# Performance work log

Hardware: AMD Instinct MI355X
Metric: run time of the kernel (lower is better)

The kernel has to match this reference:

```python
import jax, jax.numpy as jnp
import numpy as np

KH, KW = 3, 3
STRIDE = 1
PADDING = 1
CIN, COUT = 64, 64


def setup_inputs() -> dict:
    key = jax.random.key(0)
    kx, kw, kb = jax.random.split(key, 3)
    x = jax.random.normal(kx, (16, CIN, 112, 112), dtype=jnp.float32)
    # Kaiming-uniform style init, matching the torch module
    fan = CIN * KH * KW
    gain = np.sqrt(2.0)
    bound_w = np.sqrt(3.0) * gain / np.sqrt(fan)
    weights = jax.random.uniform(kw, (COUT, CIN, KH, KW), dtype=jnp.float32,
                                 minval=-bound_w, maxval=bound_w)
    bound_b = 1.0 / np.sqrt(fan)
    bias = jax.random.uniform(kb, (COUT,), dtype=jnp.float32,
                              minval=-bound_b, maxval=bound_b)
    return {"x": x, "weights": weights, "bias": bias}


def reference(x, weights, bias):
    # Equivalent to F.unfold + GEMM: a standard cross-correlation conv.
    # x: (N, C, H, W), weights: (F, C, KH, KW) -> out: (N, F, H', W')
    out = jax.lax.conv_general_dilated(
        x, weights,
        window_strides=(STRIDE, STRIDE),
        padding=((PADDING, PADDING), (PADDING, PADDING)),
        dimension_numbers=("NCHW", "OIHW", "NCHW"),
    )
    return out + bias[None, :, None, None]
```

## Files before the change

### kernel.cpp

```cpp
#include <hip/hip_runtime.h>


typedef __attribute__((ext_vector_type(8))) short bf16x8;
typedef __attribute__((ext_vector_type(4))) float f32x4;

#define CIN 64
#define COUT 64
#define HH 112
#define WW 112
#define ROWS 2
#define TILES 7
#define STRIPH (ROWS * TILES)
#define NPL 8
#define WCMAX 66
#define PLANE (8 * WCMAX * 8)
#define LDS_SHORTS (NPL * PLANE)

__device__ __forceinline__ int ladr(int pl, int oct, int w) {
    return ((pl * 8 + oct) * WCMAX + w) * 8;
}

__device__ __forceinline__ unsigned short f2bf(float f) {
    unsigned u = __builtin_bit_cast(unsigned, f);
    u += 0x7FFFu + ((u >> 16) & 1u);
    return (unsigned short)(u >> 16);
}

#if __has_builtin(__builtin_amdgcn_cvt_pk_bf16_f32)
__device__ __forceinline__ unsigned pk2bf(float a, float b) {
    typedef __attribute__((ext_vector_type(2))) __bf16 bf16x2;
    bf16x2 r = __builtin_amdgcn_cvt_pk_bf16_f32(a, b);
    return __builtin_bit_cast(unsigned, r);
}
#else
__device__ __forceinline__ unsigned pk2bf(float a, float b) {
    return (unsigned)f2bf(a) | ((unsigned)f2bf(b) << 16);
}
#endif

__global__ void conv_wprep(const float* __restrict__ w, short* __restrict__ wbf) {
    int i = blockIdx.x * 256 + threadIdx.x;
    int j = i & 7;
    int f = (i >> 3) & 63;
    int koct = (i >> 9) & 3;
    int cb = (i >> 11) & 1;
    int t = i >> 12;
    int c = cb * 32 + koct * 8 + j;
    int ky = t / 3, kx = t - ky * 3;
    wbf[i] = (short)f2bf(w[((f * CIN + c) * 3 + ky) * 3 + kx]);
}

struct StageRegs {
    float v[8][4];
    float hv;
};

__device__ __forceinline__ void stage_load(const float* __restrict__ x, int tid,
                                           int n, int c0, int W4N, int gce,
                                           int row0, StageRegs& sr)
{
    const int re  = tid >> 7;
    const int oct = (tid >> 4) & 7;
    const int w4  = tid & 15;
    const int row = row0 + re;
    sr.hv = 0.f;
#pragma unroll
    for (int k = 0; k < 8; ++k)
#pragma unroll
        for (int d = 0; d < 4; ++d) sr.v[k][d] = 0.f;
    if ((unsigned)row < (unsigned)HH && w4 < W4N) {
        const float* px = x + (((n * CIN + oct * 8) * HH + row) * WW + c0 + w4 * 4);
#pragma unroll
        for (int k = 0; k < 8; ++k) {
            const float4 t = *(const float4*)(px + k * HH * WW);
            sr.v[k][0] = t.x; sr.v[k][1] = t.y; sr.v[k][2] = t.z; sr.v[k][3] = t.w;
        }
    }
    if (tid < 128) {
        const int hrow = row0 + (tid >> 6);
        const int c = tid & 63;
        if ((unsigned)hrow < (unsigned)HH)
            sr.hv = x[((n * CIN + c) * HH + hrow) * WW + gce];
    }
}

__device__ __forceinline__ void stage_write(short* lds, int tid, int W4N,
                                            int padw, int wedge, int row0,
                                            const StageRegs& sr)
{
    const int re  = tid >> 7;
    const int oct = (tid >> 4) & 7;
    const int w4  = tid & 15;
    const int row = row0 + re;
    const int pl  = row & (NPL - 1);
    if (w4 < W4N) {
#pragma unroll
        for (int dw = 0; dw < 4; ++dw) {
            uint4 pk;
            pk.x = pk2bf(sr.v[0][dw], sr.v[1][dw]);
            pk.y = pk2bf(sr.v[2][dw], sr.v[3][dw]);
            pk.z = pk2bf(sr.v[4][dw], sr.v[5][dw]);
            pk.w = pk2bf(sr.v[6][dw], sr.v[7][dw]);
            *(uint4*)&lds[ladr(pl, oct, 1 + w4 * 4 + dw)] = pk;
        }
    }
    if (tid < 128) {
        const int hrow = row0 + (tid >> 6);
        const int c = tid & 63;
        const int hpl = hrow & (NPL - 1);
        lds[ladr(hpl, c >> 3, wedge) + (c & 7)] = (short)f2bf(sr.hv);
    }
    if (tid < 16) {
        const int prow = row0 + (tid >> 3);
        const int ppl = prow & (NPL - 1);
        *(uint4*)&lds[ladr(ppl, tid & 7, padw)] = (uint4){0u, 0u, 0u, 0u};
    }
}

__global__ __launch_bounds__(256, 1)
void conv3x3_mfma(const float* __restrict__ x, const short* __restrict__ wbf,
                  const float* __restrict__ bias, float* __restrict__ out)
{
    __shared__ __align__(16) short lds[LDS_SHORTS];
    const int tid = threadIdx.x;
    const int n = blockIdx.x;
    const int ws = blockIdx.y;
    const int strip = blockIdx.z;
    const int hb = strip * STRIPH;

    const int MTN  = ws ? 3 : 4;
    const int W4N  = ws ? 12 : 16;
    const int c0   = ws * 64;
    const int padw = ws ? 49 : 0;
    const int gce  = ws ? 63 : 64;
    const int wedge = ws ? 0 : 65;

    const int wave = tid >> 6;
    const int r  = wave >> 1;
    const int nh = wave & 1;
    const int lane = tid & 63;
    const int lm = lane & 15;
    const int q  = lane >> 4;

    StageRegs sr;

    stage_load(x, tid, n, c0, W4N, gce, hb - 1, sr);
    stage_write(lds, tid, W4N, padw, wedge, hb - 1, sr);
    stage_load(x, tid, n, c0, W4N, gce, hb + 1, sr);
    stage_write(lds, tid, W4N, padw, wedge, hb + 1, sr);

    bf16x8 bw[9][2][2];
#pragma unroll
    for (int t = 0; t < 9; ++t)
#pragma unroll
        for (int ntl = 0; ntl < 2; ++ntl) {
            const int f = (nh * 2 + ntl) * 16 + lm;
            bw[t][ntl][0] = *(const bf16x8*)(wbf + (t * 8 + q) * 512 + f * 8);
            bw[t][ntl][1] = *(const bf16x8*)(wbf + (t * 8 + 4 + q) * 512 + f * 8);
        }

    const int f0 = nh * 32 + lm;
    const float b0 = bias[f0];
    const float b1 = bias[f0 + 16];

    __syncthreads();

    for (int t = 0; t < TILES; ++t) {
        const int h0 = hb + 2 * t;
        const bool do_stage = (t < TILES - 1);

        if (do_stage) stage_load(x, tid, n, c0, W4N, gce, h0 + 3, sr);

        f32x4 acc[4][2];
#pragma unroll
        for (int mt = 0; mt < 4; ++mt)
#pragma unroll
            for (int ntl = 0; ntl < 2; ++ntl) acc[mt][ntl] = (f32x4){0.f, 0.f, 0.f, 0.f};

#pragma unroll
        for (int tap = 0; tap < 9; ++tap) {
            const int ky = tap / 3, kx = tap - ky * 3;
            const int pl = (h0 - 1 + r + ky) & (NPL - 1);
#pragma unroll
            for (int mt = 0; mt < 4; ++mt) {
                if (mt < MTN) {
                    const int wcol = mt * 16 + lm + kx;
                    const bf16x8 a0 = *(const bf16x8*)&lds[ladr(pl, q, wcol)];
                    const bf16x8 a1 = *(const bf16x8*)&lds[ladr(pl, q + 4, wcol)];
                    acc[mt][0] = __builtin_amdgcn_mfma_f32_16x16x32_bf16(a0, bw[tap][0][0], acc[mt][0], 0, 0, 0);
                    acc[mt][1] = __builtin_amdgcn_mfma_f32_16x16x32_bf16(a0, bw[tap][1][0], acc[mt][1], 0, 0, 0);
                    acc[mt][0] = __builtin_amdgcn_mfma_f32_16x16x32_bf16(a1, bw[tap][0][1], acc[mt][0], 0, 0, 0);
                    acc[mt][1] = __builtin_amdgcn_mfma_f32_16x16x32_bf16(a1, bw[tap][1][1], acc[mt][1], 0, 0, 0);
                }
            }
        }

        if (do_stage) stage_write(lds, tid, W4N, padw, wedge, h0 + 3, sr);

        const int hrow = h0 + r;
#pragma unroll
        for (int mt = 0; mt < 4; ++mt) {
            if (mt < MTN) {
#pragma unroll
                for (int ntl = 0; ntl < 2; ++ntl) {
                    const f32x4 v = acc[mt][ntl];
                    const float bb = ntl ? b1 : b0;
                    float4 s;
                    s.x = v[0] + bb; s.y = v[1] + bb; s.z = v[2] + bb; s.w = v[3] + bb;
                    *(float4*)(out + ((n * COUT + f0 + ntl * 16) * HH + hrow) * WW
                               + c0 + mt * 16 + q * 4) = s;
                }
            }
        }

        __syncthreads();
    }
}

extern "C" void kernel_launch(void* const* d_in, const int* in_sizes, int n_in,
                              void* d_out, int out_size, void* d_ws, size_t ws_size,
                              hipStream_t stream) {
    const float* x = (const float*)d_in[0];
    const float* w = (const float*)d_in[1];
    const float* b = (const float*)d_in[2];
    float* out = (float*)d_out;
    short* wbf = (short*)d_ws;

    conv_wprep<<<144, 256, 0, stream>>>(w, wbf);
    dim3 grid(16, 2, 8);
    conv3x3_mfma<<<grid, 256, 0, stream>>>(x, wbf, b, out);
}
```

Before: 124.1 us.

## Split conv tile across 8 waves, specialize staging threads, pad LDS pitch

Doubles the workgroup to 512 threads, with each wave now covering half the width tiles (mh split), so eight waves share the MFMA work per block. The staging load/write work is spread across thread ranges: threads 0-255 handle the main tile, 256-383 the halo column, and 384-399 the pad column. LDS pitch changes from 66 to 67 to reduce bank conflicts. Launch bounds move to (512,2), which caps registers per thread, and the grid is still only 256 blocks, so occupancy gains may be limited.

```diff
diff --git a/kernel.cpp b/kernel.cpp
--- a/kernel.cpp
+++ b/kernel.cpp
@@ -12,12 +12,12 @@
 #define TILES 7
 #define STRIPH (ROWS * TILES)
 #define NPL 8
-#define WCMAX 66
-#define PLANE (8 * WCMAX * 8)
-#define LDS_SHORTS (NPL * PLANE)
+#define WPITCH 67
+#define PLANE_SHORTS (8 * WPITCH * 8)
+#define LDS_SHORTS (NPL * PLANE_SHORTS)
 
 __device__ __forceinline__ int ladr(int pl, int oct, int w) {
-    return ((pl * 8 + oct) * WCMAX + w) * 8;
+    return ((pl * 8 + oct) * WPITCH + w) * 8;
 }
 
 __device__ __forceinline__ unsigned short f2bf(float f) {
@@ -51,7 +51,7 @@
 }
 
 struct StageRegs {
-    float v[8][4];
+    float4 v[8];
     float hv;
 };
 
@@ -59,28 +59,22 @@
                                            int n, int c0, int W4N, int gce,
                                            int row0, StageRegs& sr)
 {
-    const int re  = tid >> 7;
-    const int oct = (tid >> 4) & 7;
-    const int w4  = tid & 15;
-    const int row = row0 + re;
-    sr.hv = 0.f;
-#pragma unroll
-    for (int k = 0; k < 8; ++k)
-#pragma unroll
-        for (int d = 0; d < 4; ++d) sr.v[k][d] = 0.f;
-    if ((unsigned)row < (unsigned)HH && w4 < W4N) {
-        const float* px = x + (((n * CIN + oct * 8) * HH + row) * WW + c0 + w4 * 4);
-#pragma unroll
-        for (int k = 0; k < 8; ++k) {
-            const float4 t = *(const float4*)(px + k * HH * WW);
-            sr.v[k][0] = t.x; sr.v[k][1] = t.y; sr.v[k][2] = t.z; sr.v[k][3] = t.w;
-        }
-    }
-    if (tid < 128) {
-        const int hrow = row0 + (tid >> 6);
-        const int c = tid & 63;
-        if ((unsigned)hrow < (unsigned)HH)
-            sr.hv = x[((n * CIN + c) * HH + hrow) * WW + gce];
+    if (tid < 256) {
+        const int re = tid >> 7, oct = (tid >> 4) & 7, w4 = tid & 15;
+        const int row = row0 + re;
+#pragma unroll
+        for (int k = 0; k < 8; ++k) sr.v[k] = (float4){0.f, 0.f, 0.f, 0.f};
+        if ((unsigned)row < (unsigned)HH && w4 < W4N) {
+            const float* px = x + (((n * CIN + oct * 8) * HH + row) * WW + c0 + w4 * 4);
+#pragma unroll
+            for (int k = 0; k < 8; ++k) sr.v[k] = *(const float4*)(px + k * HH * WW);
+        }
+    } else if (tid < 384) {
+        const int i = tid - 256;
+        const int row = row0 + (i >> 6);
+        sr.hv = 0.f;
+        if ((unsigned)row < (unsigned)HH)
+            sr.hv = x[((n * CIN + (i & 63)) * HH + row) * WW + gce];
     }
 }
 
@@ -88,36 +82,35 @@
                                             int padw, int wedge, int row0,
                                             const StageRegs& sr)
 {
-    const int re  = tid >> 7;
-    const int oct = (tid >> 4) & 7;
-    const int w4  = tid & 15;
-    const int row = row0 + re;
-    const int pl  = row & (NPL - 1);
-    if (w4 < W4N) {
-#pragma unroll
-        for (int dw = 0; dw < 4; ++dw) {
-            uint4 pk;
-            pk.x = pk2bf(sr.v[0][dw], sr.v[1][dw]);
-            pk.y = pk2bf(sr.v[2][dw], sr.v[3][dw]);
-            pk.z = pk2bf(sr.v[4][dw], sr.v[5][dw]);
-            pk.w = pk2bf(sr.v[6][dw], sr.v[7][dw]);
-            *(uint4*)&lds[ladr(pl, oct, 1 + w4 * 4 + dw)] = pk;
-        }
+    if (tid < 256) {
+        const int re = tid >> 7, oct = (tid >> 4) & 7, w4 = tid & 15;
+        const int pl = (row0 + re) & (NPL - 1);
+        if (w4 < W4N) {
+            const float* fv = (const float*)&sr.v[0];
+#pragma unroll
+            for (int dw = 0; dw < 4; ++dw) {
+                uint4 pk;
+                pk.x = pk2bf(fv[0 * 4 + dw], fv[1 * 4 + dw]);
+                pk.y = pk2bf(fv[2 * 4 + dw], fv[3 * 4 + dw]);
+                pk.z = pk2bf(fv[4 * 4 + dw], fv[5 * 4 + dw]);
+                pk.w = pk2bf(fv[6 * 4 + dw], fv[7 * 4 + dw]);
+                *(uint4*)&lds[ladr(pl, oct, 1 + w4 * 4 + dw)] = pk;
+            }
+        }
+    } else if (tid < 384) {
+        const int i = tid - 256;
+        const int row = row0 + (i >> 6);
+        const int pl = row & (NPL - 1);
+        const int c = i & 63;
+        lds[ladr(pl, c >> 3, wedge) + (c & 7)] = (short)f2bf(sr.hv);
+    } else if (tid < 400) {
+        const int i = tid - 384;
+        const int pl = (row0 + (i >> 3)) & (NPL - 1);
+        *(uint4*)&lds[ladr(pl, i & 7, padw)] = (uint4){0u, 0u, 0u, 0u};
     }
-    if (tid < 128) {
-        const int hrow = row0 + (tid >> 6);
-        const int c = tid & 63;
-        const int hpl = hrow & (NPL - 1);
-        lds[ladr(hpl, c >> 3, wedge) + (c & 7)] = (short)f2bf(sr.hv);
-    }
-    if (tid < 16) {
-        const int prow = row0 + (tid >> 3);
-        const int ppl = prow & (NPL - 1);
-        *(uint4*)&lds[ladr(ppl, tid & 7, padw)] = (uint4){0u, 0u, 0u, 0u};
-    }
-}
-
-__global__ __launch_bounds__(256, 1)
+}
+
+__global__ __launch_bounds__(512, 2)
 void conv3x3_mfma(const float* __restrict__ x, const short* __restrict__ wbf,
                   const float* __restrict__ bias, float* __restrict__ out)
 {
@@ -125,19 +118,19 @@
     const int tid = threadIdx.x;
     const int n = blockIdx.x;
     const int ws = blockIdx.y;
-    const int strip = blockIdx.z;
-    const int hb = strip * STRIPH;
-
-    const int MTN  = ws ? 3 : 4;
-    const int W4N  = ws ? 12 : 16;
-    const int c0   = ws * 64;
-    const int padw = ws ? 49 : 0;
-    const int gce  = ws ? 63 : 64;
+    const int hb = blockIdx.z * STRIPH;
+
+    const int MTN   = ws ? 3 : 4;
+    const int W4N   = ws ? 12 : 16;
+    const int c0    = ws * 64;
+    const int padw  = ws ? 49 : 0;
+    const int gce   = ws ? 63 : 64;
     const int wedge = ws ? 0 : 65;
 
     const int wave = tid >> 6;
-    const int r  = wave >> 1;
-    const int nh = wave & 1;
+    const int r  = wave >> 2;
+    const int nh = (wave >> 1) & 1;
+    const int mh = wave & 1;
     const int lane = tid & 63;
     const int lm = lane & 15;
     const int q  = lane >> 4;
@@ -154,7 +147,7 @@
     for (int t = 0; t < 9; ++t)
 #pragma unroll
         for (int ntl = 0; ntl < 2; ++ntl) {
-            const int f = (nh * 2 + ntl) * 16 + lm;
+            const int f = nh * 32 + ntl * 16 + lm;
             bw[t][ntl][0] = *(const bf16x8*)(wbf + (t * 8 + q) * 512 + f * 8);
             bw[t][ntl][1] = *(const bf16x8*)(wbf + (t * 8 + 4 + q) * 512 + f * 8);
         }
@@ -171,26 +164,27 @@
 
         if (do_stage) stage_load(x, tid, n, c0, W4N, gce, h0 + 3, sr);
 
-        f32x4 acc[4][2];
-#pragma unroll
-        for (int mt = 0; mt < 4; ++mt)
-#pragma unroll
-            for (int ntl = 0; ntl < 2; ++ntl) acc[mt][ntl] = (f32x4){0.f, 0.f, 0.f, 0.f};
+        f32x4 acc[2][2];
+#pragma unroll
+        for (int j = 0; j < 2; ++j)
+#pragma unroll
+            for (int ntl = 0; ntl < 2; ++ntl) acc[j][ntl] = (f32x4){0.f, 0.f, 0.f, 0.f};
 
 #pragma unroll
         for (int tap = 0; tap < 9; ++tap) {
             const int ky = tap / 3, kx = tap - ky * 3;
             const int pl = (h0 - 1 + r + ky) & (NPL - 1);
 #pragma unroll
-            for (int mt = 0; mt < 4; ++mt) {
+            for (int j = 0; j < 2; ++j) {
+                const int mt = mh * 2 + j;
                 if (mt < MTN) {
                     const int wcol = mt * 16 + lm + kx;
                     const bf16x8 a0 = *(const bf16x8*)&lds[ladr(pl, q, wcol)];
                     const bf16x8 a1 = *(const bf16x8*)&lds[ladr(pl, q + 4, wcol)];
-                    acc[mt][0] = __builtin_amdgcn_mfma_f32_16x16x32_bf16(a0, bw[tap][0][0], acc[mt][0], 0, 0, 0);
-                    acc[mt][1] = __builtin_amdgcn_mfma_f32_16x16x32_bf16(a0, bw[tap][1][0], acc[mt][1], 0, 0, 0);
-                    acc[mt][0] = __builtin_amdgcn_mfma_f32_16x16x32_bf16(a1, bw[tap][0][1], acc[mt][0], 0, 0, 0);
-                    acc[mt][1] = __builtin_amdgcn_mfma_f32_16x16x32_bf16(a1, bw[tap][1][1], acc[mt][1], 0, 0, 0);
+                    acc[j][0] = __builtin_amdgcn_mfma_f32_16x16x32_bf16(a0, bw[tap][0][0], acc[j][0], 0, 0, 0);
+                    acc[j][1] = __builtin_amdgcn_mfma_f32_16x16x32_bf16(a0, bw[tap][1][0], acc[j][1], 0, 0, 0);
+                    acc[j][0] = __builtin_amdgcn_mfma_f32_16x16x32_bf16(a1, bw[tap][0][1], acc[j][0], 0, 0, 0);
+                    acc[j][1] = __builtin_amdgcn_mfma_f32_16x16x32_bf16(a1, bw[tap][1][1], acc[j][1], 0, 0, 0);
                 }
             }
         }
@@ -199,11 +193,12 @@
 
         const int hrow = h0 + r;
 #pragma unroll
-        for (int mt = 0; mt < 4; ++mt) {
+        for (int j = 0; j < 2; ++j) {
+            const int mt = mh * 2 + j;
             if (mt < MTN) {
 #pragma unroll
                 for (int ntl = 0; ntl < 2; ++ntl) {
-                    const f32x4 v = acc[mt][ntl];
+                    const f32x4 v = acc[j][ntl];
                     const float bb = ntl ? b1 : b0;
                     float4 s;
                     s.x = v[0] + bb; s.y = v[1] + bb; s.z = v[2] + bb; s.w = v[3] + bb;
@@ -228,5 +223,5 @@
 
     conv_wprep<<<144, 256, 0, stream>>>(w, wbf);
     dim3 grid(16, 2, 8);
-    conv3x3_mfma<<<grid, 256, 0, stream>>>(x, wbf, b, out);
-}
+    conv3x3_mfma<<<grid, 512, 0, stream>>>(x, wbf, b, out);
+}
```

Result: faster. 115.7 us (-6.8%).

## Shrink conv strips to four rows per block and raise occupancy

Applied to the files above, without the earlier changes.

Each block now computes 4 output rows (two 2-row tiles) instead of 14, so the grid grows from 8 to 28 strips in z. LDS shrinks to 6 fixed planes and launch bounds allow 3 blocks per CU. The aim is to fill more CUs and overlap blocks instead of relying on a long in-block rolling pipeline. In exchange, each block reloads halo rows, so the 2 extra input rows per strip now cost 50% of the 4 rows it computes instead of about 14%. An unused tile_compute helper is left behind as dead code.

```diff
diff --git a/kernel.cpp b/kernel.cpp
--- a/kernel.cpp
+++ b/kernel.cpp
@@ -8,16 +8,13 @@
 #define COUT 64
 #define HH 112
 #define WW 112
-#define ROWS 2
-#define TILES 7
-#define STRIPH (ROWS * TILES)
-#define NPL 8
-#define WCMAX 66
-#define PLANE (8 * WCMAX * 8)
-#define LDS_SHORTS (NPL * PLANE)
+#define NPL 6
+#define WPITCH 67
+#define PLANE_SHORTS (8 * WPITCH * 8)
+#define LDS_SHORTS (NPL * PLANE_SHORTS)
 
 __device__ __forceinline__ int ladr(int pl, int oct, int w) {
-    return ((pl * 8 + oct) * WCMAX + w) * 8;
+    return ((pl * 8 + oct) * WPITCH + w) * 8;
 }
 
 __device__ __forceinline__ unsigned short f2bf(float f) {
@@ -51,7 +48,7 @@
 }
 
 struct StageRegs {
-    float v[8][4];
+    float4 v[8];
     float hv;
 };
 
@@ -63,61 +60,128 @@
     const int oct = (tid >> 4) & 7;
     const int w4  = tid & 15;
     const int row = row0 + re;
+#pragma unroll
+    for (int k = 0; k < 8; ++k) sr.v[k] = (float4){0.f, 0.f, 0.f, 0.f};
     sr.hv = 0.f;
-#pragma unroll
-    for (int k = 0; k < 8; ++k)
-#pragma unroll
-        for (int d = 0; d < 4; ++d) sr.v[k][d] = 0.f;
     if ((unsigned)row < (unsigned)HH && w4 < W4N) {
         const float* px = x + (((n * CIN + oct * 8) * HH + row) * WW + c0 + w4 * 4);
 #pragma unroll
-        for (int k = 0; k < 8; ++k) {
-            const float4 t = *(const float4*)(px + k * HH * WW);
-            sr.v[k][0] = t.x; sr.v[k][1] = t.y; sr.v[k][2] = t.z; sr.v[k][3] = t.w;
-        }
-    }
-    if (tid < 128) {
-        const int hrow = row0 + (tid >> 6);
-        const int c = tid & 63;
-        if ((unsigned)hrow < (unsigned)HH)
-            sr.hv = x[((n * CIN + c) * HH + hrow) * WW + gce];
-    }
+        for (int k = 0; k < 8; ++k) sr.v[k] = *(const float4*)(px + k * HH * WW);
+    }
+    const int hrow = row0 + (tid >> 6);
+    if (tid < 128 && (unsigned)hrow < (unsigned)HH)
+        sr.hv = x[((n * CIN + (tid & 63)) * HH + hrow) * WW + gce];
 }
 
 __device__ __forceinline__ void stage_write(short* lds, int tid, int W4N,
-                                            int padw, int wedge, int row0,
+                                            int padw, int wedge, int pl0,
                                             const StageRegs& sr)
 {
     const int re  = tid >> 7;
     const int oct = (tid >> 4) & 7;
     const int w4  = tid & 15;
-    const int row = row0 + re;
-    const int pl  = row & (NPL - 1);
     if (w4 < W4N) {
+        const int pl = pl0 + re;
+        const float* fv = (const float*)&sr.v[0];
 #pragma unroll
         for (int dw = 0; dw < 4; ++dw) {
             uint4 pk;
-            pk.x = pk2bf(sr.v[0][dw], sr.v[1][dw]);
-            pk.y = pk2bf(sr.v[2][dw], sr.v[3][dw]);
-            pk.z = pk2bf(sr.v[4][dw], sr.v[5][dw]);
-            pk.w = pk2bf(sr.v[6][dw], sr.v[7][dw]);
+            pk.x = pk2bf(fv[0 * 4 + dw], fv[1 * 4 + dw]);
+            pk.y = pk2bf(fv[2 * 4 + dw], fv[3 * 4 + dw]);
+            pk.z = pk2bf(fv[4 * 4 + dw], fv[5 * 4 + dw]);
+            pk.w = pk2bf(fv[6 * 4 + dw], fv[7 * 4 + dw]);
             *(uint4*)&lds[ladr(pl, oct, 1 + w4 * 4 + dw)] = pk;
         }
     }
     if (tid < 128) {
-        const int hrow = row0 + (tid >> 6);
+        const int pl = pl0 + (tid >> 6);
         const int c = tid & 63;
-        const int hpl = hrow & (NPL - 1);
-        lds[ladr(hpl, c >> 3, wedge) + (c & 7)] = (short)f2bf(sr.hv);
+        lds[ladr(pl, c >> 3, wedge) + (c & 7)] = (short)f2bf(sr.hv);
     }
     if (tid < 16) {
-        const int prow = row0 + (tid >> 3);
-        const int ppl = prow & (NPL - 1);
-        *(uint4*)&lds[ladr(ppl, tid & 7, padw)] = (uint4){0u, 0u, 0u, 0u};
-    }
-}
-
-__global__ __launch_bounds__(256, 1)
+        const int pl = pl0 + (tid >> 3);
+        *(uint4*)&lds[ladr(pl, tid & 7, padw)] = (uint4){0u, 0u, 0u, 0u};
+    }
+}
+
+__device__ __forceinline__ void tile_compute(const short* lds,
+    const bf16x8 (&bw)[9][2], float* __restrict__ out,
+    int n, int c0, int MTN, int h0, int plbase, int lm, int q,
+    int f0, float b0, float b1)
+{
+    f32x4 acc[4][2];
+#pragma unroll
+    for (int mt = 0; mt < 4; ++mt)
+#pragma unroll
+        for (int ntl = 0; ntl < 2; ++ntl) acc[mt][ntl] = (f32x4){0.f, 0.f, 0.f, 0.f};
+
+#pragma unroll
+    for (int tap = 0; tap < 9; ++tap) {
+        const int ky = tap / 3, kx = tap - ky * 3;
+        const int pl = plbase + ky;
+#pragma unroll
+        for (int mt = 0; mt < 4; ++mt) {
+            if (mt < MTN) {
+                const int wcol = mt * 16 + lm + kx;
+                const bf16x8 a0 = *(const bf16x8*)&lds[ladr(pl, q, wcol)];
+                const bf16x8 a1 = *(const bf16x8*)&lds[ladr(pl, q + 4, wcol)];
+                acc[mt][0] = __builtin_amdgcn_mfma_f32_16x16x32_bf16(a0, bw[tap][0], acc[mt][0], 0, 0, 0);
+                acc[mt][1] = __builtin_amdgcn_mfma_f32_16x16x32_bf16(a0, bw[tap][1], acc[mt][1], 0, 0, 0);
+                const bf16x8 b2 = bw[tap][0], b3 = bw[tap][1]; (void)b2; (void)b3;
+                acc[mt][0] = acc[mt][0];
+            }
+        }
+    }
+    (void)out; (void)n; (void)c0; (void)h0; (void)lm; (void)q; (void)f0; (void)b0; (void)b1;
+}
+
+__device__ __forceinline__ void tile_run(const short* lds,
+    const bf16x8 (&bw)[9][2][2], float* __restrict__ out,
+    int n, int c0, int MTN, int h0, int plbase, int r, int lm, int q,
+    int f0, float b0, float b1)
+{
+    f32x4 acc[4][2];
+#pragma unroll
+    for (int mt = 0; mt < 4; ++mt)
+#pragma unroll
+        for (int ntl = 0; ntl < 2; ++ntl) acc[mt][ntl] = (f32x4){0.f, 0.f, 0.f, 0.f};
+
+#pragma unroll
+    for (int tap = 0; tap < 9; ++tap) {
+        const int ky = tap / 3, kx = tap - ky * 3;
+        const int pl = plbase + ky;
+#pragma unroll
+        for (int mt = 0; mt < 4; ++mt) {
+            if (mt < MTN) {
+                const int wcol = mt * 16 + lm + kx;
+                const bf16x8 a0 = *(const bf16x8*)&lds[ladr(pl, q, wcol)];
+                const bf16x8 a1 = *(const bf16x8*)&lds[ladr(pl, q + 4, wcol)];
+                acc[mt][0] = __builtin_amdgcn_mfma_f32_16x16x32_bf16(a0, bw[tap][0][0], acc[mt][0], 0, 0, 0);
+                acc[mt][1] = __builtin_amdgcn_mfma_f32_16x16x32_bf16(a0, bw[tap][1][0], acc[mt][1], 0, 0, 0);
+                acc[mt][0] = __builtin_amdgcn_mfma_f32_16x16x32_bf16(a1, bw[tap][0][1], acc[mt][0], 0, 0, 0);
+                acc[mt][1] = __builtin_amdgcn_mfma_f32_16x16x32_bf16(a1, bw[tap][1][1], acc[mt][1], 0, 0, 0);
+            }
+        }
+    }
+
+    const int hrow = h0 + r;
+#pragma unroll
+    for (int mt = 0; mt < 4; ++mt) {
+        if (mt < MTN) {
+#pragma unroll
+            for (int ntl = 0; ntl < 2; ++ntl) {
+                const f32x4 v = acc[mt][ntl];
+                const float bb = ntl ? b1 : b0;
+                float4 s;
+                s.x = v[0] + bb; s.y = v[1] + bb; s.z = v[2] + bb; s.w = v[3] + bb;
+                *(float4*)(out + ((n * COUT + f0 + ntl * 16) * HH + hrow) * WW
+                           + c0 + mt * 16 + q * 4) = s;
+            }
+        }
+    }
+}
+
+__global__ __launch_bounds__(256, 3)
 void conv3x3_mfma(const float* __restrict__ x, const short* __restrict__ wbf,
                   const float* __restrict__ bias, float* __restrict__ out)
 {
@@ -125,14 +189,13 @@
     const int tid = threadIdx.x;
     const int n = blockIdx.x;
     const int ws = blockIdx.y;
-    const int strip = blockIdx.z;
-    const int hb = strip * STRIPH;
-
-    const int MTN  = ws ? 3 : 4;
-    const int W4N  = ws ? 12 : 16;
-    const int c0   = ws * 64;
-    const int padw = ws ? 49 : 0;
-    const int gce  = ws ? 63 : 64;
+    const int hb = blockIdx.z * 4;
+
+    const int MTN   = ws ? 3 : 4;
+    const int W4N   = ws ? 12 : 16;
+    const int c0    = ws * 64;
+    const int padw  = ws ? 49 : 0;
+    const int gce   = ws ? 63 : 64;
     const int wedge = ws ? 0 : 65;
 
     const int wave = tid >> 6;
@@ -142,19 +205,20 @@
     const int lm = lane & 15;
     const int q  = lane >> 4;
 
-    StageRegs sr;
-
-    stage_load(x, tid, n, c0, W4N, gce, hb - 1, sr);
-    stage_write(lds, tid, W4N, padw, wedge, hb - 1, sr);
-    stage_load(x, tid, n, c0, W4N, gce, hb + 1, sr);
-    stage_write(lds, tid, W4N, padw, wedge, hb + 1, sr);
+    {
+        StageRegs sA, sB;
+        stage_load(x, tid, n, c0, W4N, gce, hb - 1, sA);
+        stage_load(x, tid, n, c0, W4N, gce, hb + 1, sB);
+        stage_write(lds, tid, W4N, padw, wedge, 0, sA);
+        stage_write(lds, tid, W4N, padw, wedge, 2, sB);
+    }
 
     bf16x8 bw[9][2][2];
 #pragma unroll
     for (int t = 0; t < 9; ++t)
 #pragma unroll
         for (int ntl = 0; ntl < 2; ++ntl) {
-            const int f = (nh * 2 + ntl) * 16 + lm;
+            const int f = nh * 32 + ntl * 16 + lm;
             bw[t][ntl][0] = *(const bf16x8*)(wbf + (t * 8 + q) * 512 + f * 8);
             bw[t][ntl][1] = *(const bf16x8*)(wbf + (t * 8 + 4 + q) * 512 + f * 8);
         }
@@ -165,56 +229,14 @@
 
     __syncthreads();
 
-    for (int t = 0; t < TILES; ++t) {
-        const int h0 = hb + 2 * t;
-        const bool do_stage = (t < TILES - 1);
-
-        if (do_stage) stage_load(x, tid, n, c0, W4N, gce, h0 + 3, sr);
-
-        f32x4 acc[4][2];
-#pragma unroll
-        for (int mt = 0; mt < 4; ++mt)
-#pragma unroll
-            for (int ntl = 0; ntl < 2; ++ntl) acc[mt][ntl] = (f32x4){0.f, 0.f, 0.f, 0.f};
-
-#pragma unroll
-        for (int tap = 0; tap < 9; ++tap) {
-            const int ky = tap / 3, kx = tap - ky * 3;
-            const int pl = (h0 - 1 + r + ky) & (NPL - 1);
-#pragma unroll
-            for (int mt = 0; mt < 4; ++mt) {
-                if (mt < MTN) {
-                    const int wcol = mt * 16 + lm + kx;
-                    const bf16x8 a0 = *(const bf16x8*)&lds[ladr(pl, q, wcol)];
-                    const bf16x8 a1 = *(const bf16x8*)&lds[ladr(pl, q + 4, wcol)];
-                    acc[mt][0] = __builtin_amdgcn_mfma_f32_16x16x32_bf16(a0, bw[tap][0][0], acc[mt][0], 0, 0, 0);
-                    acc[mt][1] = __builtin_amdgcn_mfma_f32_16x16x32_bf16(a0, bw[tap][1][0], acc[mt][1], 0, 0, 0);
-                    acc[mt][0] = __builtin_amdgcn_mfma_f32_16x16x32_bf16(a1, bw[tap][0][1], acc[mt][0], 0, 0, 0);
-                    acc[mt][1] = __builtin_amdgcn_mfma_f32_16x16x32_bf16(a1, bw[tap][1][1], acc[mt][1], 0, 0, 0);
-                }
-            }
-        }
-
-        if (do_stage) stage_write(lds, tid, W4N, padw, wedge, h0 + 3, sr);
-
-        const int hrow = h0 + r;
-#pragma unroll
-        for (int mt = 0; mt < 4; ++mt) {
-            if (mt < MTN) {
-#pragma unroll
-                for (int ntl = 0; ntl < 2; ++ntl) {
-                    const f32x4 v = acc[mt][ntl];
-                    const float bb = ntl ? b1 : b0;
-                    float4 s;
-                    s.x = v[0] + bb; s.y = v[1] + bb; s.z = v[2] + bb; s.w = v[3] + bb;
-                    *(float4*)(out + ((n * COUT + f0 + ntl * 16) * HH + hrow) * WW
-                               + c0 + mt * 16 + q * 4) = s;
-                }
-            }
-        }
-
-        __syncthreads();
-    }
+    StageRegs sr;
+    stage_load(x, tid, n, c0, W4N, gce, hb + 3, sr);
+    tile_run(lds, bw, out, n, c0, MTN, hb, r, r, lm, q, f0, b0, b1);
+    stage_write(lds, tid, W4N, padw, wedge, 4, sr);
+
+    __syncthreads();
+
+    tile_run(lds, bw, out, n, c0, MTN, hb + 2, r + 2, r, lm, q, f0, b0, b1);
 }
 
 extern "C" void kernel_launch(void* const* d_in, const int* in_sizes, int n_in,
@@ -227,6 +249,6 @@
     short* wbf = (short*)d_ws;
 
     conv_wprep<<<144, 256, 0, stream>>>(w, wbf);
-    dim3 grid(16, 2, 8);
+    dim3 grid(16, 2, 28);
     conv3x3_mfma<<<grid, 256, 0, stream>>>(x, wbf, b, out);
 }
```

After: 174.1 us. +40.3%, slower.
